# Kernel optimization log

Hardware: AMD Instinct MI355X
Metric: run time of the kernel (lower is better)

## Reference

```python
import jax, jax.numpy as jnp
import numpy as np

B, H, S, D = 4, 16, 2048, 128

def setup_inputs() -> dict:
    key = jax.random.key(0)
    k1, k2 = jax.random.split(key)
    x2 = jax.random.normal(k1, (B, H, S, D), dtype=jnp.float32)
    x3 = jax.random.normal(k2, (B, H, S, D), dtype=jnp.float32)
    return {"x2": x2, "x3": x3}

def reference(x2, x3):
    # scores: [B,H,S,S] = x2 @ x3^T (unscaled)
    scores = jnp.einsum('bhqd,bhkd->bhqk', x2, x3)
    probs = jax.nn.softmax(scores, axis=-1)
    # output: [B,H,S,D] = probs @ x3
    return jnp.einsum('bhqk,bhkd->bhqd', probs, x3)
```

## Files before the change

### kernel.cpp

```cpp
#include <hip/hip_runtime.h>
#include <hip/hip_bf16.h>

typedef __attribute__((ext_vector_type(4))) float f32x4;
typedef _Float16 f16;
typedef __attribute__((ext_vector_type(8))) _Float16 f16x8;
typedef __attribute__((ext_vector_type(2))) __fp16 pk16x2;
typedef __attribute__((ext_vector_type(2))) unsigned int uint2v;

#define S_LEN 2048
#define D_DIM 128
#define QBLK 128
#define KVBLK 64
#define NKV (S_LEN / KVBLK)
#define LOG2E 1.44269504088896340736f
#define EXP2(x) __builtin_amdgcn_exp2f(x)

__device__ __forceinline__ unsigned cvtpk(float a, float b) {
    union { pk16x2 p; unsigned u; } v;
    v.p = __builtin_amdgcn_cvt_pkrtz(a, b);
    return v.u;
}

__device__ __forceinline__ float hired_max(float x) {
    uint2v s = __builtin_amdgcn_permlane16_swap(__float_as_uint(x), __float_as_uint(x), false, false);
    float m = fmaxf(__uint_as_float(s.x), __uint_as_float(s.y));
    uint2v s2 = __builtin_amdgcn_permlane32_swap(__float_as_uint(m), __float_as_uint(m), false, false);
    return fmaxf(__uint_as_float(s2.x), __uint_as_float(s2.y));
}

__global__ __launch_bounds__(256, 2) void attn_kernel(
    const float* __restrict__ Q, const float* __restrict__ KV,
    float* __restrict__ Out)
{
    unsigned b = blockIdx.x;
    unsigned cpx = gridDim.x >> 3;
    unsigned work = (b & 7u) * cpx + (b >> 3);
    unsigned head = work >> 4;
    unsigned qt = work & 15u;

    const float* Qh = Q + (size_t)head * (S_LEN * D_DIM) + (size_t)qt * QBLK * D_DIM;
    const float* Kh = KV + (size_t)head * (S_LEN * D_DIM);
    float* Oh = Out + (size_t)head * (S_LEN * D_DIM) + (size_t)qt * QBLK * D_DIM;

    const int tid = threadIdx.x;
    const int wv = tid >> 6;
    const int lane = tid & 63;
    const int lo = lane & 15;
    const int hi = lane >> 4;

    __shared__ __align__(16) f16 Ksh[KVBLK * D_DIM];
    __shared__ __align__(16) f16 Vsh[D_DIM * KVBLK];

    const int srow = (tid >> 5) * 8;
    const int scol = (tid & 31) * 4;

    union { unsigned u[4]; f16x8 v; } onesu;
    onesu.u[0] = 0x3C003C00u; onesu.u[1] = 0x3C003C00u;
    onesu.u[2] = 0x3C003C00u; onesu.u[3] = 0x3C003C00u;
    const f16x8 onesf = onesu.v;

    f16x8 qf[2][4];
    #pragma unroll
    for (int t = 0; t < 2; ++t) {
        const float* qr = Qh + (wv * 32 + t * 16 + lo) * D_DIM + hi * 8;
        #pragma unroll
        for (int kc = 0; kc < 4; ++kc) {
            f32x4 a = *(const f32x4*)(qr + kc * 32);
            f32x4 c = *(const f32x4*)(qr + kc * 32 + 4);
            union { unsigned u[4]; f16x8 v; } q;
            q.u[0] = cvtpk(a[0] * LOG2E, a[1] * LOG2E);
            q.u[1] = cvtpk(a[2] * LOG2E, a[3] * LOG2E);
            q.u[2] = cvtpk(c[0] * LOG2E, c[1] * LOG2E);
            q.u[3] = cvtpk(c[2] * LOG2E, c[3] * LOG2E);
            qf[t][kc] = q.v;
        }
    }

    f32x4 oacc[2][8];
    f32x4 lacc[2];
    #pragma unroll
    for (int t = 0; t < 2; ++t) {
        #pragma unroll
        for (int n = 0; n < 8; ++n) oacc[t][n] = (f32x4){0.f, 0.f, 0.f, 0.f};
        lacc[t] = (f32x4){0.f, 0.f, 0.f, 0.f};
    }
    float mr[2] = {-1e30f, -1e30f};

    f32x4 stg[8];

    #define STAGE_LOAD(KT) do {                                               \
        const float* p_ = Kh + (size_t)(KT) * KVBLK * D_DIM + (size_t)srow * D_DIM + scol; \
        _Pragma("unroll")                                                     \
        for (int i_ = 0; i_ < 8; ++i_) stg[i_] = *(const f32x4*)(p_ + i_ * D_DIM); \
    } while (0)

    #define STAGE_WRITE() do {                                                \
        _Pragma("unroll")                                                     \
        for (int i_ = 0; i_ < 8; ++i_) {                                      \
            int row_ = srow + i_;                                             \
            int fK_ = (row_ & 7) ^ ((row_ >> 3) & 7);                         \
            uint2v w_;                                                        \
            w_.x = cvtpk(stg[i_][0], stg[i_][1]);                             \
            w_.y = cvtpk(stg[i_][2], stg[i_][3]);                             \
            *(uint2v*)&Ksh[row_ * D_DIM + (scol ^ (fK_ << 3))] = w_;          \
        }                                                                     \
        _Pragma("unroll")                                                     \
        for (int j_ = 0; j_ < 4; ++j_) {                                      \
            int d_ = scol + j_;                                               \
            int g_ = (d_ & 7) ^ ((d_ >> 3) & 7);                              \
            union { unsigned u[4]; f16x8 v; } w_;                             \
            w_.u[0] = cvtpk(stg[0][j_], stg[1][j_]);                          \
            w_.u[1] = cvtpk(stg[2][j_], stg[3][j_]);                          \
            w_.u[2] = cvtpk(stg[4][j_], stg[5][j_]);                          \
            w_.u[3] = cvtpk(stg[6][j_], stg[7][j_]);                          \
            *(f16x8*)&Vsh[d_ * KVBLK + (srow ^ (g_ << 3))] = w_.v;            \
        }                                                                     \
    } while (0)

    STAGE_LOAD(0);
    STAGE_WRITE();
    __syncthreads();

    for (int kt = 0; kt < NKV; ++kt) {
        if (kt + 1 < NKV) STAGE_LOAD(kt + 1);

        f32x4 st[2][4];
        #pragma unroll
        for (int t = 0; t < 2; ++t)
            #pragma unroll
            for (int m = 0; m < 4; ++m) st[t][m] = (f32x4){0.f, 0.f, 0.f, 0.f};
        __builtin_amdgcn_s_setprio(1);
        #pragma unroll
        for (int m = 0; m < 4; ++m) {
            int row = m * 16 + lo;
            int fK = (row & 7) ^ ((row >> 3) & 7);
            #pragma unroll
            for (int kc = 0; kc < 4; ++kc) {
                f16x8 kf = *(const f16x8*)&Ksh[row * D_DIM + ((kc * 32 + hi * 8) ^ (fK << 3))];
                st[0][m] = __builtin_amdgcn_mfma_f32_16x16x32_f16(kf, qf[0][kc], st[0][m], 0, 0, 0);
                st[1][m] = __builtin_amdgcn_mfma_f32_16x16x32_f16(kf, qf[1][kc], st[1][m], 0, 0, 0);
            }
        }
        __builtin_amdgcn_s_setprio(0);

        f16x8 pf[2][2];
        #pragma unroll
        for (int t = 0; t < 2; ++t) {
            float a0 = fmaxf(fmaxf(st[t][0][0], st[t][0][1]), st[t][0][2]);
            float a1 = fmaxf(fmaxf(st[t][0][3], st[t][1][0]), st[t][1][1]);
            float a2 = fmaxf(fmaxf(st[t][1][2], st[t][1][3]), st[t][2][0]);
            float a3 = fmaxf(fmaxf(st[t][2][1], st[t][2][2]), st[t][2][3]);
            float a4 = fmaxf(fmaxf(st[t][3][0], st[t][3][1]), st[t][3][2]);
            float b0 = fmaxf(fmaxf(a0, a1), a2);
            float b1 = fmaxf(fmaxf(a3, a4), st[t][3][3]);
            float tmax = hired_max(fmaxf(b0, b1));

            bool skip = __all(tmax - mr[t] <= 11.5415603f);
            float mnew = skip ? mr[t] : fmaxf(mr[t], tmax);

            #pragma unroll
            for (int m = 0; m < 4; ++m) {
                st[t][m][0] = EXP2(st[t][m][0] - mnew);
                st[t][m][1] = EXP2(st[t][m][1] - mnew);
                st[t][m][2] = EXP2(st[t][m][2] - mnew);
                st[t][m][3] = EXP2(st[t][m][3] - mnew);
            }

            if (!skip) {
                float scale = EXP2(mr[t] - mnew);
                float sc4[4];
                #pragma unroll
                for (int r = 0; r < 4; ++r) sc4[r] = __shfl(scale, hi * 4 + r, 64);
                #pragma unroll
                for (int n = 0; n < 8; ++n)
                    #pragma unroll
                    for (int r = 0; r < 4; ++r) oacc[t][n][r] *= sc4[r];
                #pragma unroll
                for (int r = 0; r < 4; ++r) lacc[t][r] *= sc4[r];
                mr[t] = mnew;
            }

            unsigned cc[4][2];
            #pragma unroll
            for (int m = 0; m < 4; ++m) {
                cc[m][0] = cvtpk(st[t][m][0], st[t][m][1]);
                cc[m][1] = cvtpk(st[t][m][2], st[t][m][3]);
            }
            #pragma unroll
            for (int kc2 = 0; kc2 < 2; ++kc2) {
                unsigned r0 = cc[2 * kc2][0], r1 = cc[2 * kc2][1];
                unsigned r2 = cc[2 * kc2 + 1][0], r3 = cc[2 * kc2 + 1][1];
                uint2v s02 = __builtin_amdgcn_permlane32_swap(r0, r2, false, false);
                uint2v s13 = __builtin_amdgcn_permlane32_swap(r1, r3, false, false);
                uint2v t02 = __builtin_amdgcn_permlane16_swap(s02.x, s02.y, false, false);
                uint2v t13 = __builtin_amdgcn_permlane16_swap(s13.x, s13.y, false, false);
                union { unsigned u[4]; f16x8 v; } pu;
                pu.u[0] = t02.x; pu.u[1] = t13.x; pu.u[2] = t02.y; pu.u[3] = t13.y;
                pf[t][kc2] = pu.v;
            }
        }

        __builtin_amdgcn_s_setprio(1);
        #pragma unroll
        for (int kc2 = 0; kc2 < 2; ++kc2) {
            lacc[0] = __builtin_amdgcn_mfma_f32_16x16x32_f16(pf[0][kc2], onesf, lacc[0], 0, 0, 0);
            lacc[1] = __builtin_amdgcn_mfma_f32_16x16x32_f16(pf[1][kc2], onesf, lacc[1], 0, 0, 0);
            #pragma unroll
            for (int n = 0; n < 8; ++n) {
                int d = n * 16 + lo;
                int g = (d & 7) ^ ((d >> 3) & 7);
                f16x8 vf = *(const f16x8*)&Vsh[d * KVBLK + ((kc2 * 32 + hi * 8) ^ (g << 3))];
                oacc[0][n] = __builtin_amdgcn_mfma_f32_16x16x32_f16(pf[0][kc2], vf, oacc[0][n], 0, 0, 0);
                oacc[1][n] = __builtin_amdgcn_mfma_f32_16x16x32_f16(pf[1][kc2], vf, oacc[1][n], 0, 0, 0);
            }
        }
        __builtin_amdgcn_s_setprio(0);

        __syncthreads();
        if (kt + 1 < NKV) {
            STAGE_WRITE();
            __syncthreads();
        }
    }

    #pragma unroll
    for (int t = 0; t < 2; ++t) {
        float rl[4];
        #pragma unroll
        for (int r = 0; r < 4; ++r) rl[r] = 1.0f / lacc[t][r];
        #pragma unroll
        for (int n = 0; n < 8; ++n)
            #pragma unroll
            for (int r = 0; r < 4; ++r)
                Oh[(wv * 32 + t * 16 + hi * 4 + r) * D_DIM + n * 16 + lo] = oacc[t][n][r] * rl[r];
    }
}

extern "C" void kernel_launch(void* const* d_in, const int* in_sizes, int n_in,
                              void* d_out, int out_size, void* d_ws, size_t ws_size,
                              hipStream_t stream) {
    const float* x2 = (const float*)d_in[0];
    const float* x3 = (const float*)d_in[1];
    float* out = (float*)d_out;
    dim3 grid(1024), block(256);
    hipLaunchKernelGGL(attn_kernel, grid, block, 0, stream, x2, x3, out);
}
```

Baseline: 162.8 us.

## Software-pipeline QK^T/softmax of next KV tile ahead of PV with double-buffered LDS

Double-buffers the K/V shared-memory tiles and restructures the loop so that each iteration computes QK^T and the softmax/pack for tile kt+1 before issuing the PV MFMAs for tile kt. The output and row-sum rescale is deferred until after the current PV, so the online-softmax result stays the same. The goal is to let the exp/permlane softmax work of one tile overlap with the matrix work of another and reduce MFMA idle time. In exchange, LDS use doubles and register pressure rises from holding two sets of P fragments, which may reduce occupancy.

Measured after the change: 192.5 us. 1.18x slower.

```diff
diff --git a/kernel.cpp b/kernel.cpp
--- a/kernel.cpp
+++ b/kernel.cpp
@@ -48,8 +48,8 @@
     const int lo = lane & 15;
     const int hi = lane >> 4;
 
-    __shared__ __align__(16) f16 Ksh[KVBLK * D_DIM];
-    __shared__ __align__(16) f16 Vsh[D_DIM * KVBLK];
+    __shared__ __align__(16) f16 Ksh[2][KVBLK * D_DIM];
+    __shared__ __align__(16) f16 Vsh[2][D_DIM * KVBLK];
 
     const int srow = (tid >> 5) * 8;
     const int scol = (tid & 31) * 4;
@@ -94,7 +94,7 @@
         for (int i_ = 0; i_ < 8; ++i_) stg[i_] = *(const f32x4*)(p_ + i_ * D_DIM); \
     } while (0)
 
-    #define STAGE_WRITE() do {                                                \
+    #define STAGE_WRITE(BUF) do {                                             \
         _Pragma("unroll")                                                     \
         for (int i_ = 0; i_ < 8; ++i_) {                                      \
             int row_ = srow + i_;                                             \
@@ -102,7 +102,7 @@
             uint2v w_;                                                        \
             w_.x = cvtpk(stg[i_][0], stg[i_][1]);                             \
             w_.y = cvtpk(stg[i_][2], stg[i_][3]);                             \
-            *(uint2v*)&Ksh[row_ * D_DIM + (scol ^ (fK_ << 3))] = w_;          \
+            *(uint2v*)&Ksh[BUF][row_ * D_DIM + (scol ^ (fK_ << 3))] = w_;     \
         }                                                                     \
         _Pragma("unroll")                                                     \
         for (int j_ = 0; j_ < 4; ++j_) {                                      \
@@ -113,114 +113,159 @@
             w_.u[1] = cvtpk(stg[2][j_], stg[3][j_]);                          \
             w_.u[2] = cvtpk(stg[4][j_], stg[5][j_]);                          \
             w_.u[3] = cvtpk(stg[6][j_], stg[7][j_]);                          \
-            *(f16x8*)&Vsh[d_ * KVBLK + (srow ^ (g_ << 3))] = w_.v;            \
+            *(f16x8*)&Vsh[BUF][d_ * KVBLK + (srow ^ (g_ << 3))] = w_.v;       \
         }                                                                     \
     } while (0)
 
+    #define QKT(BUF, ST) do {                                                 \
+        _Pragma("unroll")                                                     \
+        for (int t_ = 0; t_ < 2; ++t_)                                        \
+            _Pragma("unroll")                                                 \
+            for (int m_ = 0; m_ < 4; ++m_) ST[t_][m_] = (f32x4){0.f,0.f,0.f,0.f}; \
+        __builtin_amdgcn_s_setprio(1);                                        \
+        _Pragma("unroll")                                                     \
+        for (int m_ = 0; m_ < 4; ++m_) {                                      \
+            int row_ = m_ * 16 + lo;                                          \
+            int fK_ = (row_ & 7) ^ ((row_ >> 3) & 7);                         \
+            _Pragma("unroll")                                                 \
+            for (int kc_ = 0; kc_ < 4; ++kc_) {                               \
+                f16x8 kf_ = *(const f16x8*)&Ksh[BUF][row_ * D_DIM + ((kc_ * 32 + hi * 8) ^ (fK_ << 3))]; \
+                ST[0][m_] = __builtin_amdgcn_mfma_f32_16x16x32_f16(kf_, qf[0][kc_], ST[0][m_], 0, 0, 0); \
+                ST[1][m_] = __builtin_amdgcn_mfma_f32_16x16x32_f16(kf_, qf[1][kc_], ST[1][m_], 0, 0, 0); \
+            }                                                                 \
+        }                                                                     \
+        __builtin_amdgcn_s_setprio(0);                                        \
+    } while (0)
+
+    auto softmax_pack = [&](int t, f32x4 (&st)[4], f16x8 (&pfout)[2],
+                            bool &sk, float (&scp)[4]) {
+        float a0 = fmaxf(fmaxf(st[0][0], st[0][1]), st[0][2]);
+        float a1 = fmaxf(fmaxf(st[0][3], st[1][0]), st[1][1]);
+        float a2 = fmaxf(fmaxf(st[1][2], st[1][3]), st[2][0]);
+        float a3 = fmaxf(fmaxf(st[2][1], st[2][2]), st[2][3]);
+        float a4 = fmaxf(fmaxf(st[3][0], st[3][1]), st[3][2]);
+        float b0 = fmaxf(fmaxf(a0, a1), a2);
+        float b1 = fmaxf(fmaxf(a3, a4), st[3][3]);
+        float tmax = hired_max(fmaxf(b0, b1));
+
+        sk = __all(tmax - mr[t] <= 11.5415603f);
+        float mnew = sk ? mr[t] : fmaxf(mr[t], tmax);
+
+        #pragma unroll
+        for (int m = 0; m < 4; ++m) {
+            st[m][0] = EXP2(st[m][0] - mnew);
+            st[m][1] = EXP2(st[m][1] - mnew);
+            st[m][2] = EXP2(st[m][2] - mnew);
+            st[m][3] = EXP2(st[m][3] - mnew);
+        }
+        if (!sk) {
+            float scale = EXP2(mr[t] - mnew);
+            #pragma unroll
+            for (int r = 0; r < 4; ++r) scp[r] = __shfl(scale, hi * 4 + r, 64);
+            mr[t] = mnew;
+        }
+        unsigned cc[4][2];
+        #pragma unroll
+        for (int m = 0; m < 4; ++m) {
+            cc[m][0] = cvtpk(st[m][0], st[m][1]);
+            cc[m][1] = cvtpk(st[m][2], st[m][3]);
+        }
+        #pragma unroll
+        for (int kc2 = 0; kc2 < 2; ++kc2) {
+            unsigned r0 = cc[2 * kc2][0], r1 = cc[2 * kc2][1];
+            unsigned r2 = cc[2 * kc2 + 1][0], r3 = cc[2 * kc2 + 1][1];
+            uint2v s02 = __builtin_amdgcn_permlane32_swap(r0, r2, false, false);
+            uint2v s13 = __builtin_amdgcn_permlane32_swap(r1, r3, false, false);
+            uint2v t02 = __builtin_amdgcn_permlane16_swap(s02.x, s02.y, false, false);
+            uint2v t13 = __builtin_amdgcn_permlane16_swap(s13.x, s13.y, false, false);
+            union { unsigned u[4]; f16x8 v; } pu;
+            pu.u[0] = t02.x; pu.u[1] = t13.x; pu.u[2] = t02.y; pu.u[3] = t13.y;
+            pfout[kc2] = pu.v;
+        }
+    };
+
+    f16x8 pf_cur[2][2], pf_next[2][2];
+    bool sk[2]; float scp[2][4];
+
     STAGE_LOAD(0);
-    STAGE_WRITE();
+    STAGE_WRITE(0);
     __syncthreads();
-
-    for (int kt = 0; kt < NKV; ++kt) {
-        if (kt + 1 < NKV) STAGE_LOAD(kt + 1);
-
+    STAGE_LOAD(1);
+    {
         f32x4 st[2][4];
-        #pragma unroll
-        for (int t = 0; t < 2; ++t)
-            #pragma unroll
-            for (int m = 0; m < 4; ++m) st[t][m] = (f32x4){0.f, 0.f, 0.f, 0.f};
+        QKT(0, st);
+        softmax_pack(0, st[0], pf_cur[0], sk[0], scp[0]);
+        softmax_pack(1, st[1], pf_cur[1], sk[1], scp[1]);
+    }
+    STAGE_WRITE(1);
+    __syncthreads();
+
+    for (int kt = 0; kt < NKV - 1; ++kt) {
+        const int cur = kt & 1, nxt = cur ^ 1;
+        if (kt + 2 < NKV) STAGE_LOAD(kt + 2);
+
+        f32x4 st[2][4];
+        QKT(nxt, st);
+
+        softmax_pack(0, st[0], pf_next[0], sk[0], scp[0]);
+        softmax_pack(1, st[1], pf_next[1], sk[1], scp[1]);
+
         __builtin_amdgcn_s_setprio(1);
         #pragma unroll
-        for (int m = 0; m < 4; ++m) {
-            int row = m * 16 + lo;
-            int fK = (row & 7) ^ ((row >> 3) & 7);
-            #pragma unroll
-            for (int kc = 0; kc < 4; ++kc) {
-                f16x8 kf = *(const f16x8*)&Ksh[row * D_DIM + ((kc * 32 + hi * 8) ^ (fK << 3))];
-                st[0][m] = __builtin_amdgcn_mfma_f32_16x16x32_f16(kf, qf[0][kc], st[0][m], 0, 0, 0);
-                st[1][m] = __builtin_amdgcn_mfma_f32_16x16x32_f16(kf, qf[1][kc], st[1][m], 0, 0, 0);
+        for (int kc2 = 0; kc2 < 2; ++kc2) {
+            lacc[0] = __builtin_amdgcn_mfma_f32_16x16x32_f16(pf_cur[0][kc2], onesf, lacc[0], 0, 0, 0);
+            lacc[1] = __builtin_amdgcn_mfma_f32_16x16x32_f16(pf_cur[1][kc2], onesf, lacc[1], 0, 0, 0);
+            #pragma unroll
+            for (int n = 0; n < 8; ++n) {
+                int d = n * 16 + lo;
+                int g = (d & 7) ^ ((d >> 3) & 7);
+                f16x8 vf = *(const f16x8*)&Vsh[cur][d * KVBLK + ((kc2 * 32 + hi * 8) ^ (g << 3))];
+                oacc[0][n] = __builtin_amdgcn_mfma_f32_16x16x32_f16(pf_cur[0][kc2], vf, oacc[0][n], 0, 0, 0);
+                oacc[1][n] = __builtin_amdgcn_mfma_f32_16x16x32_f16(pf_cur[1][kc2], vf, oacc[1][n], 0, 0, 0);
             }
         }
         __builtin_amdgcn_s_setprio(0);
 
-        f16x8 pf[2][2];
         #pragma unroll
         for (int t = 0; t < 2; ++t) {
-            float a0 = fmaxf(fmaxf(st[t][0][0], st[t][0][1]), st[t][0][2]);
-            float a1 = fmaxf(fmaxf(st[t][0][3], st[t][1][0]), st[t][1][1]);
-            float a2 = fmaxf(fmaxf(st[t][1][2], st[t][1][3]), st[t][2][0]);
-            float a3 = fmaxf(fmaxf(st[t][2][1], st[t][2][2]), st[t][2][3]);
-            float a4 = fmaxf(fmaxf(st[t][3][0], st[t][3][1]), st[t][3][2]);
-            float b0 = fmaxf(fmaxf(a0, a1), a2);
-            float b1 = fmaxf(fmaxf(a3, a4), st[t][3][3]);
-            float tmax = hired_max(fmaxf(b0, b1));
-
-            bool skip = __all(tmax - mr[t] <= 11.5415603f);
-            float mnew = skip ? mr[t] : fmaxf(mr[t], tmax);
-
-            #pragma unroll
-            for (int m = 0; m < 4; ++m) {
-                st[t][m][0] = EXP2(st[t][m][0] - mnew);
-                st[t][m][1] = EXP2(st[t][m][1] - mnew);
-                st[t][m][2] = EXP2(st[t][m][2] - mnew);
-                st[t][m][3] = EXP2(st[t][m][3] - mnew);
-            }
-
-            if (!skip) {
-                float scale = EXP2(mr[t] - mnew);
-                float sc4[4];
-                #pragma unroll
-                for (int r = 0; r < 4; ++r) sc4[r] = __shfl(scale, hi * 4 + r, 64);
+            if (!sk[t]) {
                 #pragma unroll
                 for (int n = 0; n < 8; ++n)
                     #pragma unroll
-                    for (int r = 0; r < 4; ++r) oacc[t][n][r] *= sc4[r];
+                    for (int r = 0; r < 4; ++r) oacc[t][n][r] *= scp[t][r];
                 #pragma unroll
-                for (int r = 0; r < 4; ++r) lacc[t][r] *= sc4[r];
-                mr[t] = mnew;
+                for (int r = 0; r < 4; ++r) lacc[t][r] *= scp[t][r];
             }
-
-            unsigned cc[4][2];
-            #pragma unroll
-            for (int m = 0; m < 4; ++m) {
-                cc[m][0] = cvtpk(st[t][m][0], st[t][m][1]);
-                cc[m][1] = cvtpk(st[t][m][2], st[t][m][3]);
-            }
-            #pragma unroll
-            for (int kc2 = 0; kc2 < 2; ++kc2) {
-                unsigned r0 = cc[2 * kc2][0], r1 = cc[2 * kc2][1];
-                unsigned r2 = cc[2 * kc2 + 1][0], r3 = cc[2 * kc2 + 1][1];
-                uint2v s02 = __builtin_amdgcn_permlane32_swap(r0, r2, false, false);
-                uint2v s13 = __builtin_amdgcn_permlane32_swap(r1, r3, false, false);
-                uint2v t02 = __builtin_amdgcn_permlane16_swap(s02.x, s02.y, false, false);
-                uint2v t13 = __builtin_amdgcn_permlane16_swap(s13.x, s13.y, false, false);
-                union { unsigned u[4]; f16x8 v; } pu;
-                pu.u[0] = t02.x; pu.u[1] = t13.x; pu.u[2] = t02.y; pu.u[3] = t13.y;
-                pf[t][kc2] = pu.v;
-            }
-        }
-
+        }
+
+        __syncthreads();
+        if (kt + 2 < NKV) {
+            STAGE_WRITE(cur);
+            __syncthreads();
+        }
+        #pragma unroll
+        for (int t = 0; t < 2; ++t)
+            #pragma unroll
+            for (int kc2 = 0; kc2 < 2; ++kc2) pf_cur[t][kc2] = pf_next[t][kc2];
+    }
+
+    {
+        const int cur = (NKV - 1) & 1;
         __builtin_amdgcn_s_setprio(1);
         #pragma unroll
         for (int kc2 = 0; kc2 < 2; ++kc2) {
-            lacc[0] = __builtin_amdgcn_mfma_f32_16x16x32_f16(pf[0][kc2], onesf, lacc[0], 0, 0, 0);
-            lacc[1] = __builtin_amdgcn_mfma_f32_16x16x32_f16(pf[1][kc2], onesf, lacc[1], 0, 0, 0);
+            lacc[0] = __builtin_amdgcn_mfma_f32_16x16x32_f16(pf_cur[0][kc2], onesf, lacc[0], 0, 0, 0);
+            lacc[1] = __builtin_amdgcn_mfma_f32_16x16x32_f16(pf_cur[1][kc2], onesf, lacc[1], 0, 0, 0);
             #pragma unroll
             for (int n = 0; n < 8; ++n) {
                 int d = n * 16 + lo;
                 int g = (d & 7) ^ ((d >> 3) & 7);
-                f16x8 vf = *(const f16x8*)&Vsh[d * KVBLK + ((kc2 * 32 + hi * 8) ^ (g << 3))];
-                oacc[0][n] = __builtin_amdgcn_mfma_f32_16x16x32_f16(pf[0][kc2], vf, oacc[0][n], 0, 0, 0);
-                oacc[1][n] = __builtin_amdgcn_mfma_f32_16x16x32_f16(pf[1][kc2], vf, oacc[1][n], 0, 0, 0);
+                f16x8 vf = *(const f16x8*)&Vsh[cur][d * KVBLK + ((kc2 * 32 + hi * 8) ^ (g << 3))];
+                oacc[0][n] = __builtin_amdgcn_mfma_f32_16x16x32_f16(pf_cur[0][kc2], vf, oacc[0][n], 0, 0, 0);
+                oacc[1][n] = __builtin_amdgcn_mfma_f32_16x16x32_f16(pf_cur[1][kc2], vf, oacc[1][n], 0, 0, 0);
             }
         }
         __builtin_amdgcn_s_setprio(0);
-
-        __syncthreads();
-        if (kt + 1 < NKV) {
-            STAGE_WRITE();
-            __syncthreads();
-        }
     }
 
     #pragma unroll
```
